# Kernel tuning notes

Hardware: AMD Instinct MI355X
Metric: run time of the kernel (lower is better)

## Reference

```python
import jax, jax.numpy as jnp
import numpy as np

B, C, H, W = 4, 256, 64, 64
CH = C // 2


def setup_inputs() -> dict:
    key = jax.random.key(0)
    ks = jax.random.split(key, 8)
    s_in = 1.0 / np.sqrt(C)  # conv2d default init scale (fan_in = C for 1x1)
    return {
        "a": jax.random.normal(ks[0], (B, C, H, W), dtype=jnp.float32),
        "p": jax.random.normal(ks[1], (B, C, H, W), dtype=jnp.float32),
        "Wq": jax.random.uniform(ks[2], (CH, C), jnp.float32, -s_in, s_in),
        "bq": jax.random.uniform(ks[3], (CH,), jnp.float32, -s_in, s_in),
        "Wk": jax.random.uniform(ks[4], (CH, C), jnp.float32, -s_in, s_in),
        "bk": jax.random.uniform(ks[5], (CH,), jnp.float32, -s_in, s_in),
        "Wv": jax.random.uniform(ks[6], (C, C), jnp.float32, -s_in, s_in),
        "bv": jax.random.uniform(ks[7], (C,), jnp.float32, -s_in, s_in),
    }


def reference(a, p, Wq, bq, Wk, bk, Wv, bv):
    b, c, h, w = a.shape
    hw = h * w
    # 1x1 convs == per-pixel channel matmuls; flatten spatial dims to hw
    Q = jnp.einsum('oc,bchw->bohw', Wq, a).reshape(b, -1, hw) + bq[None, :, None]   # [B, C/2, HW]
    K = jnp.einsum('oc,bchw->bohw', Wk, p).reshape(b, -1, hw) + bk[None, :, None]   # [B, C/2, HW]
    V = jnp.einsum('oc,bchw->bohw', Wv, p).reshape(b, -1, hw) + bv[None, :, None]   # [B, C,   HW]
    # attn[b,m,n] = softmax_n( Q[:, :, m] . K[:, :, n] )
    attn = jax.nn.softmax(jnp.einsum('bcm,bcn->bmn', Q, K), axis=-1)                # [B, HW, HW]
    # out[b,c,m] = sum_n V[b,c,n] * attn[b,m,n]  (V @ attn^T)
    out = jnp.einsum('bcn,bmn->bcm', V, attn).reshape(b, c, h, w)
    return out + a
```

## Files before the change

kernel.cpp:

```cpp
#include <hip/hip_runtime.h>
#include <stdint.h>

#define B_ 4
#define C_ 256
#define CH_ 128
#define HW_ 4096
#define L2E 1.44269504f
#define SHIFT_L2 14.4269504f

typedef __bf16 bf16;
typedef __bf16 v8bf __attribute__((ext_vector_type(8)));
typedef __bf16 v4bf __attribute__((ext_vector_type(4)));
typedef float v4f __attribute__((ext_vector_type(4)));
struct f4 { float x, y, z, w; };
struct f2 { float x, y; };

#define GAS __attribute__((address_space(1)))
#define LAS __attribute__((address_space(3)))

__device__ __forceinline__ void async_copy16(const void* gptr, void* lptr) {
  __builtin_amdgcn_global_load_lds((GAS void*)gptr, (LAS void*)lptr, 16, 0, 0);
}

__global__ __launch_bounds__(512)
void proj_kernel(const float* __restrict__ a, const float* __restrict__ p,
                 const float* __restrict__ Wq, const float* __restrict__ bq,
                 const float* __restrict__ Wk, const float* __restrict__ bk,
                 const float* __restrict__ Wv, const float* __restrict__ bv,
                 bf16* __restrict__ Qt, bf16* __restrict__ Kt, bf16* __restrict__ Vn)
{
  __shared__ bf16 Xt[64 * 272];
  __shared__ bf16 Ds[9216];

  const int t = threadIdx.x;
  const int lane = t & 63;
  const int w = t >> 6;
  const int l15 = lane & 15;
  const int q = lane >> 4;

  const int s0 = blockIdx.x * 64;
  const int b = blockIdx.y;
  const int z = blockIdx.z;

  const float* X = (z == 0) ? a : p;
  const float* W; const float* bias;
  if (z == 0)      { W = Wq; bias = bq; }
  else if (z == 1) { W = Wk; bias = bk; }
  else             { W = Wv + (size_t)(z - 2) * 128 * C_; bias = bv + (z - 2) * 128; }

  const float* Xb = X + ((size_t)b * C_) * HW_;
  #pragma unroll
  for (int j = 0; j < 8; ++j) {
    int linear = t + 512 * j;
    int s = (linear & 31) * 2;
    int cp = linear >> 5;
    f2 x0 = *(const f2*)&Xb[(size_t)(2 * cp) * HW_ + s0 + s];
    f2 x1 = *(const f2*)&Xb[(size_t)(2 * cp + 1) * HW_ + s0 + s];
    unsigned short u00 = __builtin_bit_cast(unsigned short, (bf16)x0.x);
    unsigned short u01 = __builtin_bit_cast(unsigned short, (bf16)x0.y);
    unsigned short u10 = __builtin_bit_cast(unsigned short, (bf16)x1.x);
    unsigned short u11 = __builtin_bit_cast(unsigned short, (bf16)x1.y);
    *(unsigned int*)&Xt[(s + 0) * 272 + 2 * cp] = (unsigned int)u00 | ((unsigned int)u10 << 16);
    *(unsigned int*)&Xt[(s + 1) * 272 + 2 * cp] = (unsigned int)u01 | ((unsigned int)u11 << 16);
  }

  v8bf Af[8];
  const float* Wrow = W + (size_t)(16 * w + l15) * C_;
  #pragma unroll
  for (int kk = 0; kk < 8; ++kk) {
    f4 f0 = *(const f4*)&Wrow[kk * 32 + q * 8];
    f4 f1 = *(const f4*)&Wrow[kk * 32 + q * 8 + 4];
    v8bf f;
    f[0] = (bf16)f0.x; f[1] = (bf16)f0.y; f[2] = (bf16)f0.z; f[3] = (bf16)f0.w;
    f[4] = (bf16)f1.x; f[5] = (bf16)f1.y; f[6] = (bf16)f1.z; f[7] = (bf16)f1.w;
    Af[kk] = f;
  }

  __syncthreads();

  v4f acc[4];
  #pragma unroll
  for (int ns = 0; ns < 4; ++ns) { v4f zz = {0.f, 0.f, 0.f, 0.f}; acc[ns] = zz; }
  #pragma unroll
  for (int ns = 0; ns < 4; ++ns)
    #pragma unroll
    for (int kk = 0; kk < 8; ++kk) {
      v8bf Bf = *(const v8bf*)&Xt[(16 * ns + l15) * 272 + kk * 32 + q * 8];
      acc[ns] = __builtin_amdgcn_mfma_f32_16x16x32_bf16(Af[kk], Bf, acc[ns], 0, 0, 0);
    }

  if (z < 2) {
    #pragma unroll
    for (int ns = 0; ns < 4; ++ns)
      #pragma unroll
      for (int r = 0; r < 4; ++r)
        Ds[(16 * ns + l15) * 144 + 16 * w + 4 * q + r] =
            (bf16)(acc[ns][r] + bias[16 * w + 4 * q + r]);
    __syncthreads();
    bf16* dst = (z == 0) ? Qt : Kt;
    #pragma unroll
    for (int i = 0; i < 2; ++i) {
      int idx = t + 512 * i;
      int s = idx >> 4, ch = (idx & 15) * 8;
      *(v8bf*)&dst[((size_t)b * HW_ + s0 + s) * CH_ + ch] = *(const v8bf*)&Ds[s * 144 + ch];
    }
  } else {
    int o0 = (z - 2) * 128;
    #pragma unroll
    for (int ns = 0; ns < 4; ++ns)
      #pragma unroll
      for (int r = 0; r < 4; ++r) {
        int pos = 32 * (ns >> 1) + 8 * (l15 >> 2) + 4 * (ns & 1) + (l15 & 3);
        Ds[(16 * w + 4 * q + r) * 72 + pos] =
            (bf16)(acc[ns][r] + bias[16 * w + 4 * q + r]);
      }
    __syncthreads();
    #pragma unroll
    for (int i = 0; i < 2; ++i) {
      int idx = t + 512 * i;
      int o = idx >> 3, ch = (idx & 7) * 8;
      *(v8bf*)&Vn[((size_t)b * C_ + o0 + o) * HW_ + s0 + ch] = *(const v8bf*)&Ds[o * 72 + ch];
    }
  }
}

#define BUFSZ 49920
#define LDS_K 0
#define LDS_V 16640
#define TSTRIDE 52
#define TREGION 13312
#define LDS_TOTAL 99840

__global__ __launch_bounds__(512, 2)
void attn_kernel(const bf16* __restrict__ Qt, const bf16* __restrict__ Kt,
                 const bf16* __restrict__ Vn, const float* __restrict__ a,
                 float* __restrict__ out, bf16* __restrict__ Op,
                 float* __restrict__ Ls, int nsplit)
{
  extern __shared__ char smem[];
  const int t = threadIdx.x;
  const int lane = t & 63;
  const int w = t >> 6;
  const int l15 = lane & 15;
  const int q = lane >> 4;

  const int Lhw = blockIdx.x + 16 * (blockIdx.y + 4 * blockIdx.z);
  const int cpx = 8 * nsplit;
  const int logical = (Lhw & 7) * cpx + (Lhw >> 3);
  const int m0 = (logical & 15) * 256;
  const int gg = logical >> 4;
  const int b = gg & 3;
  const int sp = gg >> 2;

  v8bf Qf[2][4];
  #pragma unroll
  for (int s = 0; s < 2; ++s) {
    const bf16* qrow = Qt + ((size_t)b * HW_ + m0 + 32 * w + 16 * s + l15) * CH_;
    #pragma unroll
    for (int kk = 0; kk < 4; ++kk)
      Qf[s][kk] = *(const v8bf*)&qrow[kk * 32 + q * 8];
  }

  v4f O[2][16];
  #pragma unroll
  for (int s = 0; s < 2; ++s)
    #pragma unroll
    for (int cs = 0; cs < 16; ++cs) { v4f zz = {0.f, 0.f, 0.f, 0.f}; O[s][cs] = zz; }
  float lsum[2] = {0.f, 0.f};

  const bf16* Kb = Kt + (size_t)b * HW_ * CH_;
  const bf16* Vb = Vn + (size_t)b * C_ * HW_;

  const int NT = 64 / nsplit;
  const int t0 = sp * NT;

  auto stage = [&](int tile, int bsel) {
    char* base = smem + bsel * BUFSZ;
    int n0 = tile * 64;
    #pragma unroll
    for (int j = 0; j < 2; ++j) {
      int i = 8 * j + w;
      async_copy16(Kb + ((size_t)(n0 + i + 16 * q)) * CH_ + l15 * 8, base + LDS_K + i * 1040);
    }
    #pragma unroll
    for (int j = 0; j < 4; ++j) {
      int i = 8 * j + w;
      async_copy16(Vb + ((size_t)(i + 32 * (lane >> 3))) * HW_ + n0 + (lane & 7) * 8,
                   base + LDS_V + i * 1040);
    }
  };

  stage(t0, 0);
  __syncthreads();

  int cur = 0;
  for (int nt = 0; nt < NT; ++nt) {
    if (nt + 1 < NT) stage(t0 + nt + 1, cur ^ 1);

    const char* Kbase = smem + cur * BUFSZ + LDS_K;
    const char* Vbase = smem + cur * BUFSZ + LDS_V;

    v4f St[4][2];
    #pragma unroll
    for (int sub = 0; sub < 4; ++sub)
      #pragma unroll
      for (int s = 0; s < 2; ++s) { v4f zz = {0.f, 0.f, 0.f, 0.f}; St[sub][s] = zz; }
    #pragma unroll
    for (int sub = 0; sub < 4; ++sub)
      #pragma unroll
      for (int kk = 0; kk < 4; ++kk) {
        v8bf Kf = *(const v8bf*)(Kbase + l15 * 1040 + sub * 256 + kk * 64 + q * 16);
        St[sub][0] = __builtin_amdgcn_mfma_f32_16x16x32_bf16(Kf, Qf[0][kk], St[sub][0], 0, 0, 0);
        St[sub][1] = __builtin_amdgcn_mfma_f32_16x16x32_bf16(Kf, Qf[1][kk], St[sub][1], 0, 0, 0);
      }

    v8bf Pf[2][2];
    #pragma unroll
    for (int s = 0; s < 2; ++s) {
      float ls = 0.f;
      #pragma unroll
      for (int kk = 0; kk < 2; ++kk)
        #pragma unroll
        for (int a2 = 0; a2 < 2; ++a2)
          #pragma unroll
          for (int r = 0; r < 4; ++r) {
            float pv = exp2f(St[2 * kk + a2][s][r] * L2E - SHIFT_L2);
            Pf[s][kk][4 * a2 + r] = (bf16)pv;
            ls += pv;
          }
      lsum[s] += ls;
    }

    #pragma unroll
    for (int cs = 0; cs < 16; ++cs)
      #pragma unroll
      for (int kk = 0; kk < 2; ++kk) {
        v8bf Vf = *(const v8bf*)(Vbase +
                                 (16 * (cs & 1) + l15) * 1040 + (cs >> 1) * 128 + kk * 64 + q * 16);
        O[0][cs] = __builtin_amdgcn_mfma_f32_16x16x32_bf16(Pf[0][kk], Vf, O[0][cs], 0, 0, 0);
        O[1][cs] = __builtin_amdgcn_mfma_f32_16x16x32_bf16(Pf[1][kk], Vf, O[1][cs], 0, 0, 0);
      }

    __syncthreads();
    cur ^= 1;
  }

  float lfin[2];
  #pragma unroll
  for (int s = 0; s < 2; ++s) {
    float l = lsum[s];
    l += __shfl_xor(l, 16);
    l += __shfl_xor(l, 32);
    lfin[s] = l;
  }

  if (nsplit > 1 && lane < 16) {
    #pragma unroll
    for (int s = 0; s < 2; ++s)
      Ls[((size_t)sp * B_ + b) * HW_ + m0 + 32 * w + 16 * s + lane] = lfin[s];
  }

  float linv[2][4];
  #pragma unroll
  for (int s = 0; s < 2; ++s)
    #pragma unroll
    for (int r = 0; r < 4; ++r)
      linv[s][r] = (nsplit == 1) ? 1.0f / __shfl(lfin[s], 4 * q + r) : 1.0f;

  bf16* T = (bf16*)smem;
  for (int round = 0; round < 4; ++round) {
    __syncthreads();
    if ((w >> 1) == round) {
      bf16* Tw = T + (w & 1) * TREGION;
      #pragma unroll
      for (int s = 0; s < 2; ++s)
        #pragma unroll
        for (int cs = 0; cs < 16; ++cs) {
          v4bf pp4;
          #pragma unroll
          for (int r = 0; r < 4; ++r) pp4[r] = (bf16)(O[s][cs][r] * linv[s][r]);
          *(v4bf*)&Tw[(16 * cs + l15) * TSTRIDE + 16 * s + 4 * q] = pp4;
        }
    }
    __syncthreads();
    #pragma unroll
    for (int it = 0; it < 4; ++it) {
      int idx = t + 512 * it;
      int tt = idx >> 10;
      int c = (idx >> 2) & 255;
      int mc = idx & 3;
      int wavew = round * 2 + tt;
      int mg = m0 + 32 * wavew + mc * 8;
      const bf16* Trow = &T[tt * TREGION + c * TSTRIDE + mc * 8];
      v4bf lo = *(const v4bf*)&Trow[0];
      v4bf hi = *(const v4bf*)&Trow[4];
      if (nsplit == 1) {
        size_t gi = ((size_t)b * C_ + c) * HW_ + mg;
        #pragma unroll
        for (int j2 = 0; j2 < 4; ++j2) out[gi + j2] = (float)lo[j2] + a[gi + j2];
        #pragma unroll
        for (int j2 = 0; j2 < 4; ++j2) out[gi + 4 + j2] = (float)hi[j2] + a[gi + 4 + j2];
      } else {
        size_t gi = (((size_t)sp * B_ + b) * C_ + c) * HW_ + mg;
        v8bf val;
        #pragma unroll
        for (int j2 = 0; j2 < 4; ++j2) { val[j2] = lo[j2]; val[4 + j2] = hi[j2]; }
        *(v8bf*)&Op[gi] = val;
      }
    }
  }
}

__global__ __launch_bounds__(256)
void combine_kernel(const bf16* __restrict__ Op, const float* __restrict__ Ls,
                    const float* __restrict__ a, float* __restrict__ out, int nsplit)
{
  int idx = blockIdx.x * 256 + threadIdx.x;
  int m4 = (idx & (HW_ / 4 - 1)) * 4;
  int bc = idx >> 10;
  int b = bc >> 8;

  float a0 = 0.f, a1 = 0.f, a2 = 0.f, a3 = 0.f;
  float L0 = 0.f, L1 = 0.f, L2 = 0.f, L3 = 0.f;
  for (int s = 0; s < nsplit; ++s) {
    v4bf o = *(const v4bf*)&Op[((size_t)s * B_ * C_ + bc) * HW_ + m4];
    f4 lp = *(const f4*)&Ls[((size_t)s * B_ + b) * HW_ + m4];
    a0 += (float)o[0]; a1 += (float)o[1]; a2 += (float)o[2]; a3 += (float)o[3];
    L0 += lp.x; L1 += lp.y; L2 += lp.z; L3 += lp.w;
  }
  f4 av = *(const f4*)&a[(size_t)bc * HW_ + m4];
  f4 ov;
  ov.x = a0 / L0 + av.x;
  ov.y = a1 / L1 + av.y;
  ov.z = a2 / L2 + av.z;
  ov.w = a3 / L3 + av.w;
  *(f4*)&out[(size_t)bc * HW_ + m4] = ov;
}

extern "C" void kernel_launch(void* const* d_in, const int* in_sizes, int n_in,
                              void* d_out, int out_size, void* d_ws, size_t ws_size,
                              hipStream_t stream) {
  const float* a  = (const float*)d_in[0];
  const float* p  = (const float*)d_in[1];
  const float* Wq = (const float*)d_in[2];
  const float* bq = (const float*)d_in[3];
  const float* Wk = (const float*)d_in[4];
  const float* bk = (const float*)d_in[5];
  const float* Wv = (const float*)d_in[6];
  const float* bv = (const float*)d_in[7];
  float* out = (float*)d_out;

  bf16* Qt = (bf16*)d_ws;
  bf16* Kt = Qt + (size_t)B_ * HW_ * CH_;
  bf16* Vn = Kt + (size_t)B_ * HW_ * CH_;

  const size_t proj_bytes = 16777216ull;
  const size_t part_bytes = (size_t)B_ * C_ * HW_ * 2;
  const size_t stat_bytes = (size_t)B_ * HW_ * 4;
  auto need = [&](int S) { return proj_bytes + (size_t)S * (part_bytes + stat_bytes); };

  int S;
  if      (ws_size >= need(4)) S = 4;
  else if (ws_size >= need(2)) S = 2;
  else                         S = 1;

  bf16* Op = (bf16*)((char*)d_ws + proj_bytes);
  float* Ls = (float*)((char*)d_ws + proj_bytes + (size_t)S * part_bytes);

  static bool attr_done = false;
  if (!attr_done) {
    hipFuncSetAttribute((const void*)attn_kernel,
                        hipFuncAttributeMaxDynamicSharedMemorySize, LDS_TOTAL);
    attr_done = true;
  }

  dim3 pg(HW_ / 64, B_, 4);
  proj_kernel<<<pg, 512, 0, stream>>>(a, p, Wq, bq, Wk, bk, Wv, bv, Qt, Kt, Vn);

  dim3 ag(HW_ / 256, B_, S);
  attn_kernel<<<ag, 512, LDS_TOTAL, stream>>>(Qt, Kt, Vn, a, out, Op, Ls, S);

  if (S > 1) {
    int nblk = (B_ * C_ * HW_ / 4) / 256;
    combine_kernel<<<nblk, 256, 0, stream>>>(Op, Ls, a, out, S);
  }
}
```

Before: 174.0 us.

## Fuse projection, attention and combine into one cooperative persistent kernel

```diff
diff --git a/kernel.cpp b/kernel.cpp
--- a/kernel.cpp
+++ b/kernel.cpp
@@ -1,5 +1,8 @@
 #include <hip/hip_runtime.h>
+#include <hip/hip_cooperative_groups.h>
 #include <stdint.h>
+
+namespace cg = cooperative_groups;
 
 #define B_ 4
 #define C_ 256
@@ -22,33 +25,16 @@
   __builtin_amdgcn_global_load_lds((GAS void*)gptr, (LAS void*)lptr, 16, 0, 0);
 }
 
-__global__ __launch_bounds__(512)
-void proj_kernel(const float* __restrict__ a, const float* __restrict__ p,
-                 const float* __restrict__ Wq, const float* __restrict__ bq,
-                 const float* __restrict__ Wk, const float* __restrict__ bk,
-                 const float* __restrict__ Wv, const float* __restrict__ bv,
-                 bf16* __restrict__ Qt, bf16* __restrict__ Kt, bf16* __restrict__ Vn)
-{
-  __shared__ bf16 Xt[64 * 272];
-  __shared__ bf16 Ds[9216];
-
+#define BUFSZ 49920
+#define LDS_K 0
+#define LDS_V 16640
+#define TSTRIDE 52
+#define TREGION 13312
+#define LDS_TOTAL 99840
+
+__device__ __forceinline__ void proj_stageX(const float* __restrict__ Xb, int s0,
+                                            bf16* __restrict__ Xt) {
   const int t = threadIdx.x;
-  const int lane = t & 63;
-  const int w = t >> 6;
-  const int l15 = lane & 15;
-  const int q = lane >> 4;
-
-  const int s0 = blockIdx.x * 64;
-  const int b = blockIdx.y;
-  const int z = blockIdx.z;
-
-  const float* X = (z == 0) ? a : p;
-  const float* W; const float* bias;
-  if (z == 0)      { W = Wq; bias = bq; }
-  else if (z == 1) { W = Wk; bias = bk; }
-  else             { W = Wv + (size_t)(z - 2) * 128 * C_; bias = bv + (z - 2) * 128; }
-
-  const float* Xb = X + ((size_t)b * C_) * HW_;
   #pragma unroll
   for (int j = 0; j < 8; ++j) {
     int linear = t + 512 * j;
@@ -63,6 +49,19 @@
     *(unsigned int*)&Xt[(s + 0) * 272 + 2 * cp] = (unsigned int)u00 | ((unsigned int)u10 << 16);
     *(unsigned int*)&Xt[(s + 1) * 272 + 2 * cp] = (unsigned int)u01 | ((unsigned int)u11 << 16);
   }
+}
+
+__device__ __forceinline__ void proj_pass(const bf16* __restrict__ Xt,
+                                          bf16* __restrict__ Ds,
+                                          const float* __restrict__ W,
+                                          const float* __restrict__ bias,
+                                          bool vmode, bf16* __restrict__ dst,
+                                          int s0, int b, int o0) {
+  const int t = threadIdx.x;
+  const int lane = t & 63;
+  const int w = t >> 6;
+  const int l15 = lane & 15;
+  const int q = lane >> 4;
 
   v8bf Af[8];
   const float* Wrow = W + (size_t)(16 * w + l15) * C_;
@@ -76,8 +75,6 @@
     Af[kk] = f;
   }
 
-  __syncthreads();
-
   v4f acc[4];
   #pragma unroll
   for (int ns = 0; ns < 4; ++ns) { v4f zz = {0.f, 0.f, 0.f, 0.f}; acc[ns] = zz; }
@@ -89,7 +86,8 @@
       acc[ns] = __builtin_amdgcn_mfma_f32_16x16x32_bf16(Af[kk], Bf, acc[ns], 0, 0, 0);
     }
 
-  if (z < 2) {
+  __syncthreads();
+  if (!vmode) {
     #pragma unroll
     for (int ns = 0; ns < 4; ++ns)
       #pragma unroll
@@ -97,7 +95,6 @@
         Ds[(16 * ns + l15) * 144 + 16 * w + 4 * q + r] =
             (bf16)(acc[ns][r] + bias[16 * w + 4 * q + r]);
     __syncthreads();
-    bf16* dst = (z == 0) ? Qt : Kt;
     #pragma unroll
     for (int i = 0; i < 2; ++i) {
       int idx = t + 512 * i;
@@ -105,7 +102,6 @@
       *(v8bf*)&dst[((size_t)b * HW_ + s0 + s) * CH_ + ch] = *(const v8bf*)&Ds[s * 144 + ch];
     }
   } else {
-    int o0 = (z - 2) * 128;
     #pragma unroll
     for (int ns = 0; ns < 4; ++ns)
       #pragma unroll
@@ -119,23 +115,19 @@
     for (int i = 0; i < 2; ++i) {
       int idx = t + 512 * i;
       int o = idx >> 3, ch = (idx & 7) * 8;
-      *(v8bf*)&Vn[((size_t)b * C_ + o0 + o) * HW_ + s0 + ch] = *(const v8bf*)&Ds[o * 72 + ch];
-    }
-  }
-}
-
-#define BUFSZ 49920
-#define LDS_K 0
-#define LDS_V 16640
-#define TSTRIDE 52
-#define TREGION 13312
-#define LDS_TOTAL 99840
+      *(v8bf*)&dst[((size_t)b * C_ + o0 + o) * HW_ + s0 + ch] = *(const v8bf*)&Ds[o * 72 + ch];
+    }
+  }
+}
 
 __global__ __launch_bounds__(512, 2)
-void attn_kernel(const bf16* __restrict__ Qt, const bf16* __restrict__ Kt,
-                 const bf16* __restrict__ Vn, const float* __restrict__ a,
-                 float* __restrict__ out, bf16* __restrict__ Op,
-                 float* __restrict__ Ls, int nsplit)
+void fused_kernel(const float* __restrict__ a, const float* __restrict__ p,
+                  const float* __restrict__ Wq, const float* __restrict__ bq,
+                  const float* __restrict__ Wk, const float* __restrict__ bk,
+                  const float* __restrict__ Wv, const float* __restrict__ bv,
+                  bf16* __restrict__ Qt, bf16* __restrict__ Kt,
+                  bf16* __restrict__ Vn, float* __restrict__ out,
+                  bf16* __restrict__ Op, float* __restrict__ Ls, int nsplit)
 {
   extern __shared__ char smem[];
   const int t = threadIdx.x;
@@ -144,197 +136,218 @@
   const int l15 = lane & 15;
   const int q = lane >> 4;
 
-  const int Lhw = blockIdx.x + 16 * (blockIdx.y + 4 * blockIdx.z);
-  const int cpx = 8 * nsplit;
-  const int logical = (Lhw & 7) * cpx + (Lhw >> 3);
-  const int m0 = (logical & 15) * 256;
-  const int gg = logical >> 4;
-  const int b = gg & 3;
-  const int sp = gg >> 2;
-
-  v8bf Qf[2][4];
-  #pragma unroll
-  for (int s = 0; s < 2; ++s) {
-    const bf16* qrow = Qt + ((size_t)b * HW_ + m0 + 32 * w + 16 * s + l15) * CH_;
-    #pragma unroll
-    for (int kk = 0; kk < 4; ++kk)
-      Qf[s][kk] = *(const v8bf*)&qrow[kk * 32 + q * 8];
-  }
-
-  v4f O[2][16];
-  #pragma unroll
-  for (int s = 0; s < 2; ++s)
-    #pragma unroll
-    for (int cs = 0; cs < 16; ++cs) { v4f zz = {0.f, 0.f, 0.f, 0.f}; O[s][cs] = zz; }
-  float lsum[2] = {0.f, 0.f};
-
-  const bf16* Kb = Kt + (size_t)b * HW_ * CH_;
-  const bf16* Vb = Vn + (size_t)b * C_ * HW_;
-
-  const int NT = 64 / nsplit;
-  const int t0 = sp * NT;
-
-  auto stage = [&](int tile, int bsel) {
-    char* base = smem + bsel * BUFSZ;
-    int n0 = tile * 64;
-    #pragma unroll
-    for (int j = 0; j < 2; ++j) {
-      int i = 8 * j + w;
-      async_copy16(Kb + ((size_t)(n0 + i + 16 * q)) * CH_ + l15 * 8, base + LDS_K + i * 1040);
-    }
-    #pragma unroll
-    for (int j = 0; j < 4; ++j) {
-      int i = 8 * j + w;
-      async_copy16(Vb + ((size_t)(i + 32 * (lane >> 3))) * HW_ + n0 + (lane & 7) * 8,
-                   base + LDS_V + i * 1040);
-    }
-  };
-
-  stage(t0, 0);
-  __syncthreads();
-
-  int cur = 0;
-  for (int nt = 0; nt < NT; ++nt) {
-    if (nt + 1 < NT) stage(t0 + nt + 1, cur ^ 1);
-
-    const char* Kbase = smem + cur * BUFSZ + LDS_K;
-    const char* Vbase = smem + cur * BUFSZ + LDS_V;
-
-    v4f St[4][2];
-    #pragma unroll
-    for (int sub = 0; sub < 4; ++sub)
-      #pragma unroll
-      for (int s = 0; s < 2; ++s) { v4f zz = {0.f, 0.f, 0.f, 0.f}; St[sub][s] = zz; }
-    #pragma unroll
-    for (int sub = 0; sub < 4; ++sub)
-      #pragma unroll
-      for (int kk = 0; kk < 4; ++kk) {
-        v8bf Kf = *(const v8bf*)(Kbase + l15 * 1040 + sub * 256 + kk * 64 + q * 16);
-        St[sub][0] = __builtin_amdgcn_mfma_f32_16x16x32_bf16(Kf, Qf[0][kk], St[sub][0], 0, 0, 0);
-        St[sub][1] = __builtin_amdgcn_mfma_f32_16x16x32_bf16(Kf, Qf[1][kk], St[sub][1], 0, 0, 0);
-      }
-
-    v8bf Pf[2][2];
+  {
+    bf16* Xt = (bf16*)smem;
+    bf16* Ds = (bf16*)(smem + 34816);
+    for (int u = blockIdx.x; u < 256; u += gridDim.x) {
+      const int s0 = (u & 63) * 64;
+      const int b = u >> 6;
+      proj_stageX(a + ((size_t)b * C_) * HW_, s0, Xt);
+      __syncthreads();
+      proj_pass(Xt, Ds, Wq, bq, false, Qt, s0, b, 0);
+      __syncthreads();
+      proj_stageX(p + ((size_t)b * C_) * HW_, s0, Xt);
+      __syncthreads();
+      proj_pass(Xt, Ds, Wk, bk, false, Kt, s0, b, 0);
+      proj_pass(Xt, Ds, Wv, bv, true, Vn, s0, b, 0);
+      proj_pass(Xt, Ds, Wv + (size_t)128 * C_, bv + 128, true, Vn, s0, b, 128);
+      __syncthreads();
+    }
+  }
+
+  cg::this_grid().sync();
+
+  {
+    const int bid = blockIdx.x;
+    const int m0 = (bid & 15) * 256;
+    const int b = (bid >> 4) & 3;
+    const int sp = bid >> 6;
+
+    v8bf Qf[2][4];
     #pragma unroll
     for (int s = 0; s < 2; ++s) {
-      float ls = 0.f;
-      #pragma unroll
-      for (int kk = 0; kk < 2; ++kk)
-        #pragma unroll
-        for (int a2 = 0; a2 < 2; ++a2)
-          #pragma unroll
-          for (int r = 0; r < 4; ++r) {
-            float pv = exp2f(St[2 * kk + a2][s][r] * L2E - SHIFT_L2);
-            Pf[s][kk][4 * a2 + r] = (bf16)pv;
-            ls += pv;
+      const bf16* qrow = Qt + ((size_t)b * HW_ + m0 + 32 * w + 16 * s + l15) * CH_;
+      #pragma unroll
+      for (int kk = 0; kk < 4; ++kk)
+        Qf[s][kk] = *(const v8bf*)&qrow[kk * 32 + q * 8];
+    }
+
+    v4f O[2][16];
+    #pragma unroll
+    for (int s = 0; s < 2; ++s)
+      #pragma unroll
+      for (int cs = 0; cs < 16; ++cs) { v4f zz = {0.f, 0.f, 0.f, 0.f}; O[s][cs] = zz; }
+    float lsum[2] = {0.f, 0.f};
+
+    const bf16* Kb = Kt + (size_t)b * HW_ * CH_;
+    const bf16* Vb = Vn + (size_t)b * C_ * HW_;
+
+    const int NT = 64 / nsplit;
+    const int t0 = sp * NT;
+
+    auto stage = [&](int tile, int bsel) {
+      char* base = smem + bsel * BUFSZ;
+      int n0 = tile * 64;
+      #pragma unroll
+      for (int j = 0; j < 2; ++j) {
+        int i = 8 * j + w;
+        async_copy16(Kb + ((size_t)(n0 + i + 16 * q)) * CH_ + l15 * 8, base + LDS_K + i * 1040);
+      }
+      #pragma unroll
+      for (int j = 0; j < 4; ++j) {
+        int i = 8 * j + w;
+        async_copy16(Vb + ((size_t)(i + 32 * (lane >> 3))) * HW_ + n0 + (lane & 7) * 8,
+                     base + LDS_V + i * 1040);
+      }
+    };
+
+    stage(t0, 0);
+    __syncthreads();
+
+    int cur = 0;
+    for (int nt = 0; nt < NT; ++nt) {
+      if (nt + 1 < NT) stage(t0 + nt + 1, cur ^ 1);
+
+      const char* Kbase = smem + cur * BUFSZ + LDS_K;
+      const char* Vbase = smem + cur * BUFSZ + LDS_V;
+
+      v4f St[4][2];
+      #pragma unroll
+      for (int sub = 0; sub < 4; ++sub)
+        #pragma unroll
+        for (int s = 0; s < 2; ++s) { v4f zz = {0.f, 0.f, 0.f, 0.f}; St[sub][s] = zz; }
+      #pragma unroll
+      for (int sub = 0; sub < 4; ++sub)
+        #pragma unroll
+        for (int kk = 0; kk < 4; ++kk) {
+          v8bf Kf = *(const v8bf*)(Kbase + l15 * 1040 + sub * 256 + kk * 64 + q * 16);
+          St[sub][0] = __builtin_amdgcn_mfma_f32_16x16x32_bf16(Kf, Qf[0][kk], St[sub][0], 0, 0, 0);
+          St[sub][1] = __builtin_amdgcn_mfma_f32_16x16x32_bf16(Kf, Qf[1][kk], St[sub][1], 0, 0, 0);
+        }
+
+      v8bf Pf[2][2];
+      #pragma unroll
+      for (int s = 0; s < 2; ++s) {
+        float ls = 0.f;
+        #pragma unroll
+        for (int kk = 0; kk < 2; ++kk)
+          #pragma unroll
+          for (int a2 = 0; a2 < 2; ++a2)
+            #pragma unroll
+            for (int r = 0; r < 4; ++r) {
+              float pv = exp2f(St[2 * kk + a2][s][r] * L2E - SHIFT_L2);
+              Pf[s][kk][4 * a2 + r] = (bf16)pv;
+              ls += pv;
+            }
+        lsum[s] += ls;
+      }
+
+      #pragma unroll
+      for (int cs = 0; cs < 16; ++cs)
+        #pragma unroll
+        for (int kk = 0; kk < 2; ++kk) {
+          v8bf Vf = *(const v8bf*)(Vbase +
+                                   (16 * (cs & 1) + l15) * 1040 + (cs >> 1) * 128 + kk * 64 + q * 16);
+          O[0][cs] = __builtin_amdgcn_mfma_f32_16x16x32_bf16(Pf[0][kk], Vf, O[0][cs], 0, 0, 0);
+          O[1][cs] = __builtin_amdgcn_mfma_f32_16x16x32_bf16(Pf[1][kk], Vf, O[1][cs], 0, 0, 0);
+        }
+
+      __syncthreads();
+      cur ^= 1;
+    }
+
+    float lfin[2];
+    #pragma unroll
+    for (int s = 0; s < 2; ++s) {
+      float l = lsum[s];
+      l += __shfl_xor(l, 16);
+      l += __shfl_xor(l, 32);
+      lfin[s] = l;
+    }
+
+    if (nsplit > 1 && lane < 16) {
+      #pragma unroll
+      for (int s = 0; s < 2; ++s)
+        Ls[((size_t)sp * B_ + b) * HW_ + m0 + 32 * w + 16 * s + lane] = lfin[s];
+    }
+
+    float linv[2][4];
+    #pragma unroll
+    for (int s = 0; s < 2; ++s)
+      #pragma unroll
+      for (int r = 0; r < 4; ++r)
+        linv[s][r] = (nsplit == 1) ? 1.0f / __shfl(lfin[s], 4 * q + r) : 1.0f;
+
+    bf16* T = (bf16*)smem;
+    for (int round = 0; round < 4; ++round) {
+      __syncthreads();
+      if ((w >> 1) == round) {
+        bf16* Tw = T + (w & 1) * TREGION;
+        #pragma unroll
+        for (int s = 0; s < 2; ++s)
+          #pragma unroll
+          for (int cs = 0; cs < 16; ++cs) {
+            v4bf pp4;
+            #pragma unroll
+            for (int r = 0; r < 4; ++r) pp4[r] = (bf16)(O[s][cs][r] * linv[s][r]);
+            *(v4bf*)&Tw[(16 * cs + l15) * TSTRIDE + 16 * s + 4 * q] = pp4;
           }
-      lsum[s] += ls;
-    }
-
-    #pragma unroll
-    for (int cs = 0; cs < 16; ++cs)
-      #pragma unroll
-      for (int kk = 0; kk < 2; ++kk) {
-        v8bf Vf = *(const v8bf*)(Vbase +
-                                 (16 * (cs & 1) + l15) * 1040 + (cs >> 1) * 128 + kk * 64 + q * 16);
-        O[0][cs] = __builtin_amdgcn_mfma_f32_16x16x32_bf16(Pf[0][kk], Vf, O[0][cs], 0, 0, 0);
-        O[1][cs] = __builtin_amdgcn_mfma_f32_16x16x32_bf16(Pf[1][kk], Vf, O[1][cs], 0, 0, 0);
-      }
-
-    __syncthreads();
-    cur ^= 1;
-  }
-
-  float lfin[2];
-  #pragma unroll
-  for (int s = 0; s < 2; ++s) {
-    float l = lsum[s];
-    l += __shfl_xor(l, 16);
-    l += __shfl_xor(l, 32);
-    lfin[s] = l;
-  }
-
-  if (nsplit > 1 && lane < 16) {
-    #pragma unroll
-    for (int s = 0; s < 2; ++s)
-      Ls[((size_t)sp * B_ + b) * HW_ + m0 + 32 * w + 16 * s + lane] = lfin[s];
-  }
-
-  float linv[2][4];
-  #pragma unroll
-  for (int s = 0; s < 2; ++s)
-    #pragma unroll
-    for (int r = 0; r < 4; ++r)
-      linv[s][r] = (nsplit == 1) ? 1.0f / __shfl(lfin[s], 4 * q + r) : 1.0f;
-
-  bf16* T = (bf16*)smem;
-  for (int round = 0; round < 4; ++round) {
-    __syncthreads();
-    if ((w >> 1) == round) {
-      bf16* Tw = T + (w & 1) * TREGION;
-      #pragma unroll
-      for (int s = 0; s < 2; ++s)
-        #pragma unroll
-        for (int cs = 0; cs < 16; ++cs) {
-          v4bf pp4;
-          #pragma unroll
-          for (int r = 0; r < 4; ++r) pp4[r] = (bf16)(O[s][cs][r] * linv[s][r]);
-          *(v4bf*)&Tw[(16 * cs + l15) * TSTRIDE + 16 * s + 4 * q] = pp4;
+      }
+      __syncthreads();
+      #pragma unroll
+      for (int it = 0; it < 4; ++it) {
+        int idx = t + 512 * it;
+        int tt = idx >> 10;
+        int c = (idx >> 2) & 255;
+        int mc = idx & 3;
+        int wavew = round * 2 + tt;
+        int mg = m0 + 32 * wavew + mc * 8;
+        const bf16* Trow = &T[tt * TREGION + c * TSTRIDE + mc * 8];
+        v4bf lo = *(const v4bf*)&Trow[0];
+        v4bf hi = *(const v4bf*)&Trow[4];
+        if (nsplit == 1) {
+          size_t gi = ((size_t)b * C_ + c) * HW_ + mg;
+          #pragma unroll
+          for (int j2 = 0; j2 < 4; ++j2) out[gi + j2] = (float)lo[j2] + a[gi + j2];
+          #pragma unroll
+          for (int j2 = 0; j2 < 4; ++j2) out[gi + 4 + j2] = (float)hi[j2] + a[gi + 4 + j2];
+        } else {
+          size_t gi = (((size_t)sp * B_ + b) * C_ + c) * HW_ + mg;
+          v8bf val;
+          #pragma unroll
+          for (int j2 = 0; j2 < 4; ++j2) { val[j2] = lo[j2]; val[4 + j2] = hi[j2]; }
+          *(v8bf*)&Op[gi] = val;
         }
-    }
-    __syncthreads();
-    #pragma unroll
-    for (int it = 0; it < 4; ++it) {
-      int idx = t + 512 * it;
-      int tt = idx >> 10;
-      int c = (idx >> 2) & 255;
-      int mc = idx & 3;
-      int wavew = round * 2 + tt;
-      int mg = m0 + 32 * wavew + mc * 8;
-      const bf16* Trow = &T[tt * TREGION + c * TSTRIDE + mc * 8];
-      v4bf lo = *(const v4bf*)&Trow[0];
-      v4bf hi = *(const v4bf*)&Trow[4];
-      if (nsplit == 1) {
-        size_t gi = ((size_t)b * C_ + c) * HW_ + mg;
-        #pragma unroll
-        for (int j2 = 0; j2 < 4; ++j2) out[gi + j2] = (float)lo[j2] + a[gi + j2];
-        #pragma unroll
-        for (int j2 = 0; j2 < 4; ++j2) out[gi + 4 + j2] = (float)hi[j2] + a[gi + 4 + j2];
-      } else {
-        size_t gi = (((size_t)sp * B_ + b) * C_ + c) * HW_ + mg;
-        v8bf val;
-        #pragma unroll
-        for (int j2 = 0; j2 < 4; ++j2) { val[j2] = lo[j2]; val[4 + j2] = hi[j2]; }
-        *(v8bf*)&Op[gi] = val;
-      }
-    }
-  }
-}
-
-__global__ __launch_bounds__(256)
-void combine_kernel(const bf16* __restrict__ Op, const float* __restrict__ Ls,
-                    const float* __restrict__ a, float* __restrict__ out, int nsplit)
-{
-  int idx = blockIdx.x * 256 + threadIdx.x;
-  int m4 = (idx & (HW_ / 4 - 1)) * 4;
-  int bc = idx >> 10;
-  int b = bc >> 8;
-
-  float a0 = 0.f, a1 = 0.f, a2 = 0.f, a3 = 0.f;
-  float L0 = 0.f, L1 = 0.f, L2 = 0.f, L3 = 0.f;
-  for (int s = 0; s < nsplit; ++s) {
-    v4bf o = *(const v4bf*)&Op[((size_t)s * B_ * C_ + bc) * HW_ + m4];
-    f4 lp = *(const f4*)&Ls[((size_t)s * B_ + b) * HW_ + m4];
-    a0 += (float)o[0]; a1 += (float)o[1]; a2 += (float)o[2]; a3 += (float)o[3];
-    L0 += lp.x; L1 += lp.y; L2 += lp.z; L3 += lp.w;
-  }
-  f4 av = *(const f4*)&a[(size_t)bc * HW_ + m4];
-  f4 ov;
-  ov.x = a0 / L0 + av.x;
-  ov.y = a1 / L1 + av.y;
-  ov.z = a2 / L2 + av.z;
-  ov.w = a3 / L3 + av.w;
-  *(f4*)&out[(size_t)bc * HW_ + m4] = ov;
+      }
+    }
+  }
+
+  if (nsplit > 1) {
+    cg::this_grid().sync();
+
+    const int nthreads = gridDim.x * 512;
+    for (int idx = blockIdx.x * 512 + t; idx < B_ * C_ * HW_ / 4; idx += nthreads) {
+      int m4 = (idx & (HW_ / 4 - 1)) * 4;
+      int bc = idx >> 10;
+      int b = bc >> 8;
+
+      float a0 = 0.f, a1 = 0.f, a2 = 0.f, a3 = 0.f;
+      float L0 = 0.f, L1 = 0.f, L2 = 0.f, L3 = 0.f;
+      for (int s = 0; s < nsplit; ++s) {
+        v4bf o = *(const v4bf*)&Op[((size_t)s * B_ * C_ + bc) * HW_ + m4];
+        f4 lp = *(const f4*)&Ls[((size_t)s * B_ + b) * HW_ + m4];
+        a0 += (float)o[0]; a1 += (float)o[1]; a2 += (float)o[2]; a3 += (float)o[3];
+        L0 += lp.x; L1 += lp.y; L2 += lp.z; L3 += lp.w;
+      }
+      f4 av = *(const f4*)&a[(size_t)bc * HW_ + m4];
+      f4 ov;
+      ov.x = a0 / L0 + av.x;
+      ov.y = a1 / L1 + av.y;
+      ov.z = a2 / L2 + av.z;
+      ov.w = a3 / L3 + av.w;
+      *(f4*)&out[(size_t)bc * HW_ + m4] = ov;
+    }
+  }
 }
 
 extern "C" void kernel_launch(void* const* d_in, const int* in_sizes, int n_in,
@@ -369,19 +382,14 @@
 
   static bool attr_done = false;
   if (!attr_done) {
-    hipFuncSetAttribute((const void*)attn_kernel,
+    hipFuncSetAttribute((const void*)fused_kernel,
                         hipFuncAttributeMaxDynamicSharedMemorySize, LDS_TOTAL);
     attr_done = true;
   }
 
-  dim3 pg(HW_ / 64, B_, 4);
-  proj_kernel<<<pg, 512, 0, stream>>>(a, p, Wq, bq, Wk, bk, Wv, bv, Qt, Kt, Vn);
-
-  dim3 ag(HW_ / 256, B_, S);
-  attn_kernel<<<ag, 512, LDS_TOTAL, stream>>>(Qt, Kt, Vn, a, out, Op, Ls, S);
-
-  if (S > 1) {
-    int nblk = (B_ * C_ * HW_ / 4) / 256;
-    combine_kernel<<<nblk, 256, 0, stream>>>(Op, Ls, a, out, S);
-  }
-}
+  void* args[] = {(void*)&a, (void*)&p, (void*)&Wq, (void*)&bq, (void*)&Wk,
+                  (void*)&bk, (void*)&Wv, (void*)&bv, (void*)&Qt, (void*)&Kt,
+                  (void*)&Vn, (void*)&out, (void*)&Op, (void*)&Ls, (void*)&S};
+  hipLaunchCooperativeKernel((const void*)fused_kernel,
+                             dim3(64 * S), dim3(512), args, LDS_TOTAL, stream);
+}
```

Measured after the change: 264.5 us. 1.52x slower.
